# Kernel tuning notes

Hardware: AMD Instinct MI355X
Metric: run time of the kernel (lower is better)

The kernel has to match this reference:

```python
import jax, jax.numpy as jnp
import numpy as np

D_IN, H1, H2, N_CLS, BATCH = 1024, 2048, 2048, 1000, 8192


def setup_inputs() -> dict:
    key = jax.random.key(0)
    ks = jax.random.split(key, 7)
    x = jax.random.normal(ks[0], (BATCH, D_IN), dtype=jnp.float32)
    # torch.nn.Linear default init scale ~ 1/sqrt(fan_in); weights stored [out, in]
    W1 = jax.random.normal(ks[1], (H1, D_IN), dtype=jnp.float32) / np.sqrt(D_IN).astype(np.float32)
    b1 = jax.random.normal(ks[2], (H1,), dtype=jnp.float32) * 0.01
    W2 = jax.random.normal(ks[3], (H2, H1), dtype=jnp.float32) / np.sqrt(H1).astype(np.float32)
    b2 = jax.random.normal(ks[4], (H2,), dtype=jnp.float32) * 0.01
    W3 = jax.random.normal(ks[5], (N_CLS, H2), dtype=jnp.float32) / np.sqrt(H2).astype(np.float32)
    b3 = jax.random.normal(ks[6], (N_CLS,), dtype=jnp.float32) * 0.01
    return {"x": x, "W1": W1, "b1": b1, "W2": W2, "b2": b2, "W3": W3, "b3": b3}


def reference(x, W1, b1, W2, b2, W3, b3):
    # forward_with_coactivations: classifier = [Linear, ReLU, Linear, ReLU, Linear]
    # activation points: the two ReLU layers and the final Linear.
    prev_act = (x > 0).astype(jnp.float32)  # [B, D_IN]

    z1 = x @ W1.T + b1                      # [B, H1]
    a1 = jax.nn.relu(z1)
    act1 = (z1 > 0).astype(jnp.float32)     # (relu(z)>0) == (z>0)
    # sum_s outer(prev_act[s], act1[s]) == prev_act.T @ act1
    coact0 = jnp.einsum('bi,bj->ij', prev_act, act1)  # [D_IN, H1]

    z2 = a1 @ W2.T + b2                     # [B, H2]
    a2 = jax.nn.relu(z2)
    act2 = (z2 > 0).astype(jnp.float32)
    coact1 = jnp.einsum('bi,bj->ij', act1, act2)      # [H1, H2]

    logits = a2 @ W3.T + b3                 # [B, N_CLS]
    act3 = (logits > 0).astype(jnp.float32)
    coact2 = jnp.einsum('bi,bj->ij', act2, act3)      # [H2, N_CLS]

    return logits, coact0, coact1, coact2
```

## Files before the change

### kernel.cpp

```cpp
#include <hip/hip_runtime.h>
#include <hip/hip_bf16.h>


typedef short v8s __attribute__((ext_vector_type(8)));
typedef float v4f __attribute__((ext_vector_type(4)));
typedef int v4i __attribute__((ext_vector_type(4)));

enum { MODE_RELU = 0, MODE_LOGITS = 1 };

__device__ __forceinline__ void async_cp16(const void* gsrc, void* ldst) {
  __builtin_amdgcn_global_load_lds(
      (const __attribute__((address_space(1))) void*)gsrc,
      (__attribute__((address_space(3))) void*)ldst, 16, 0, 0);
}

template <int MODE>
__global__ __launch_bounds__(256) void gemm_nt(
    const __hip_bfloat16* __restrict__ A, const __hip_bfloat16* __restrict__ B,
    const float* __restrict__ bias, void* __restrict__ Cout,
    int M, int N, int K, int n_store, int ldc) {
  __shared__ __hip_bfloat16 sA[128 * 64];
  __shared__ __hip_bfloat16 sB[128 * 64];
  const int t = threadIdx.x;
  const int m0 = blockIdx.y * 128;
  const int n0 = blockIdx.x * 128;

  const __hip_bfloat16* aG[4];
  const __hip_bfloat16* bG[4];
  char* lA[4];
  char* lB[4];
#pragma unroll
  for (int j = 0; j < 4; j++) {
    const int c = j * 256 + t;
    const int row = c >> 3;
    const int g = (c & 7) ^ (row & 7);
    aG[j] = A + (size_t)(m0 + row) * K + g * 8;
    bG[j] = B + (size_t)(n0 + row) * K + g * 8;
    lA[j] = (char*)sA + c * 16;
    lB[j] = (char*)sB + c * 16;
  }

  const int lane = t & 63;
  const int wave = t >> 6;
  const int wm = (wave & 1) * 64;
  const int wn = (wave >> 1) * 64;
  const int lrow = lane & 15;
  const int quad = lane >> 4;

  const int g0 = quad ^ (lrow & 7);
  const __hip_bfloat16* pa0 = sA + (wm + lrow) * 64 + g0 * 8;
  const __hip_bfloat16* pa1 = sA + (wm + lrow) * 64 + (g0 ^ 4) * 8;
  const __hip_bfloat16* pb0 = sB + (wn + lrow) * 64 + g0 * 8;
  const __hip_bfloat16* pb1 = sB + (wn + lrow) * 64 + (g0 ^ 4) * 8;

  v4f acc[4][4] = {};

  for (int k0 = 0; k0 < K; k0 += 64) {
#pragma unroll
    for (int j = 0; j < 4; j++) {
      async_cp16(aG[j] + k0, lA[j]);
      async_cp16(bG[j] + k0, lB[j]);
    }
    __syncthreads();

    v8s a0[4], b0[4], a1[4], b1[4];
#pragma unroll
    for (int i = 0; i < 4; i++) {
      a0[i] = *(const v8s*)(pa0 + i * 16 * 64);
      b0[i] = *(const v8s*)(pb0 + i * 16 * 64);
    }
#pragma unroll
    for (int mi = 0; mi < 4; mi++)
#pragma unroll
      for (int ni = 0; ni < 4; ni++)
        acc[mi][ni] = __builtin_amdgcn_mfma_f32_16x16x32_bf16(
            a0[mi], b0[ni], acc[mi][ni], 0, 0, 0);
#pragma unroll
    for (int i = 0; i < 4; i++) {
      a1[i] = *(const v8s*)(pa1 + i * 16 * 64);
      b1[i] = *(const v8s*)(pb1 + i * 16 * 64);
    }
#pragma unroll
    for (int mi = 0; mi < 4; mi++)
#pragma unroll
      for (int ni = 0; ni < 4; ni++)
        acc[mi][ni] = __builtin_amdgcn_mfma_f32_16x16x32_bf16(
            a1[mi], b1[ni], acc[mi][ni], 0, 0, 0);
    __syncthreads();
  }

#pragma unroll
  for (int ni = 0; ni < 4; ni++) {
    const int col = n0 + wn + ni * 16 + lrow;
    float bv = 0.f;
    if (MODE == MODE_RELU) bv = bias[col];
    if (MODE == MODE_LOGITS && col < n_store) bv = bias[col];
#pragma unroll
    for (int mi = 0; mi < 4; mi++) {
      const int rowb = m0 + wm + mi * 16 + quad * 4;
#pragma unroll
      for (int r = 0; r < 4; r++) {
        const int row = rowb + r;
        const float v = acc[mi][ni][r] + bv;
        if (MODE == MODE_RELU) {
          ((__hip_bfloat16*)Cout)[(size_t)row * ldc + col] =
              __float2bfloat16(v > 0.f ? v : 0.f);
        } else {
          if (col < n_store)
            ((float*)Cout)[(size_t)row * ldc + col] = v;
        }
      }
    }
  }
}

__global__ __launch_bounds__(256) void gemm_nt_i8(
    const char* __restrict__ A, const char* __restrict__ B,
    float* __restrict__ P, int M, int N, int Kc, int n_store, size_t slice) {
  __shared__ char sA[128 * 128];
  __shared__ char sB[128 * 128];
  const int t = threadIdx.x;
  const int m0 = blockIdx.y * 128;
  const int n0 = blockIdx.x * 128;
  const int kbeg = blockIdx.z * Kc;
  const int kend = kbeg + Kc;
  const size_t K = (size_t)Kc * gridDim.z;
  float* __restrict__ Pz = P + (size_t)blockIdx.z * slice;

  const char* aG[4];
  const char* bG[4];
  char* lA[4];
  char* lB[4];
#pragma unroll
  for (int j = 0; j < 4; j++) {
    const int c = j * 256 + t;
    const int row = c >> 3;
    const int g = (c & 7) ^ (row & 7);
    aG[j] = A + (size_t)(m0 + row) * K + g * 16;
    bG[j] = B + (size_t)(n0 + row) * K + g * 16;
    lA[j] = sA + c * 16;
    lB[j] = sB + c * 16;
  }

  const int lane = t & 63;
  const int wave = t >> 6;
  const int wm = (wave & 1) * 64;
  const int wn = (wave >> 1) * 64;
  const int lrow = lane & 15;
  const int quad = lane >> 4;

  const int g0 = quad ^ (lrow & 7);
  const char* pa0 = sA + (wm + lrow) * 128 + g0 * 16;
  const char* pa1 = sA + (wm + lrow) * 128 + (g0 ^ 4) * 16;
  const char* pb0 = sB + (wn + lrow) * 128 + g0 * 16;
  const char* pb1 = sB + (wn + lrow) * 128 + (g0 ^ 4) * 16;

  v4i acc[4][4] = {};

  for (int k0 = kbeg; k0 < kend; k0 += 128) {
#pragma unroll
    for (int j = 0; j < 4; j++) {
      async_cp16(aG[j] + k0, lA[j]);
      async_cp16(bG[j] + k0, lB[j]);
    }
    __syncthreads();

    v4i a0[4], b0[4], a1[4], b1[4];
#pragma unroll
    for (int i = 0; i < 4; i++) {
      a0[i] = *(const v4i*)(pa0 + i * 16 * 128);
      b0[i] = *(const v4i*)(pb0 + i * 16 * 128);
    }
#pragma unroll
    for (int mi = 0; mi < 4; mi++)
#pragma unroll
      for (int ni = 0; ni < 4; ni++)
        acc[mi][ni] = __builtin_amdgcn_mfma_i32_16x16x64_i8(
            a0[mi], b0[ni], acc[mi][ni], 0, 0, 0);
#pragma unroll
    for (int i = 0; i < 4; i++) {
      a1[i] = *(const v4i*)(pa1 + i * 16 * 128);
      b1[i] = *(const v4i*)(pb1 + i * 16 * 128);
    }
#pragma unroll
    for (int mi = 0; mi < 4; mi++)
#pragma unroll
      for (int ni = 0; ni < 4; ni++)
        acc[mi][ni] = __builtin_amdgcn_mfma_i32_16x16x64_i8(
            a1[mi], b1[ni], acc[mi][ni], 0, 0, 0);
    __syncthreads();
  }

#pragma unroll
  for (int ni = 0; ni < 4; ni++) {
    const int col = n0 + wn + ni * 16 + lrow;
    if (col >= n_store) continue;
#pragma unroll
    for (int mi = 0; mi < 4; mi++) {
      const int rowb = m0 + wm + mi * 16 + quad * 4;
#pragma unroll
      for (int r = 0; r < 4; r++) {
        Pz[(size_t)(rowb + r) * n_store + col] = (float)acc[mi][ni][r];
      }
    }
  }
}

template <int Z>
__global__ __launch_bounds__(256) void reduce_part(
    const float* __restrict__ P, float* __restrict__ out, int n4, size_t slice) {
  const int i = blockIdx.x * 256 + threadIdx.x;
  if (i >= n4) return;
  float4 s = ((const float4*)P)[i];
#pragma unroll
  for (int z = 1; z < Z; z++) {
    const float4 v = ((const float4*)(P + (size_t)z * slice))[i];
    s.x += v.x; s.y += v.y; s.z += v.z; s.w += v.w;
  }
  ((float4*)out)[i] = s;
}

__device__ __forceinline__ float tofl(float v) { return v; }
__device__ __forceinline__ float tofl(__hip_bfloat16 v) { return __bfloat162float(v); }

template <typename Tin>
__global__ __launch_bounds__(256) void transpose_bin8(
    const Tin* __restrict__ in, char* __restrict__ out,
    int R, int ldin, int Cphys) {
  __shared__ char tile[64][65];
  const int c0 = blockIdx.x * 64;
  const int r0 = blockIdx.y * 64;
  const int tx = threadIdx.x & 63;
  const int ty = threadIdx.x >> 6;
#pragma unroll
  for (int i = 0; i < 64; i += 4) {
    const int c = c0 + tx;
    const int r = r0 + ty + i;
    float v = 0.f;
    if (c < Cphys) v = tofl(in[(size_t)r * ldin + c]);
    tile[ty + i][tx] = (v > 0.f) ? 1 : 0;
  }
  __syncthreads();
  const int u = threadIdx.x & 15;
  const int cg = threadIdx.x >> 4;
#pragma unroll
  for (int i = 0; i < 64; i += 16) {
    const int col = cg + i;
    char4 v;
    v.x = tile[4 * u + 0][col];
    v.y = tile[4 * u + 1][col];
    v.z = tile[4 * u + 2][col];
    v.w = tile[4 * u + 3][col];
    *(char4*)&out[(size_t)(c0 + col) * R + r0 + 4 * u] = v;
  }
}

struct Cvt4 {
  const float* src[4];
  __hip_bfloat16* dst[4];
  int n4[4];
};
__global__ __launch_bounds__(256) void f32_to_bf16_multi(Cvt4 c) {
  int i = blockIdx.x * 256 + threadIdx.x;
#pragma unroll
  for (int s = 0; s < 4; s++) {
    if (i < c.n4[s]) {
      const float4 v = ((const float4*)c.src[s])[i];
      union { __hip_bfloat16 h[4]; ushort4 u; } cv;
      cv.h[0] = __float2bfloat16(v.x);
      cv.h[1] = __float2bfloat16(v.y);
      cv.h[2] = __float2bfloat16(v.z);
      cv.h[3] = __float2bfloat16(v.w);
      ((ushort4*)c.dst[s])[i] = cv.u;
      return;
    }
    i -= c.n4[s];
  }
}

extern "C" void kernel_launch(void* const* d_in, const int* in_sizes, int n_in,
                              void* d_out, int out_size, void* d_ws, size_t ws_size,
                              hipStream_t stream) {
  const float* x  = (const float*)d_in[0];
  const float* W1 = (const float*)d_in[1];
  const float* b1 = (const float*)d_in[2];
  const float* W2 = (const float*)d_in[3];
  const float* b2 = (const float*)d_in[4];
  const float* W3 = (const float*)d_in[5];
  const float* b3 = (const float*)d_in[6];

  float* logits = (float*)d_out;
  float* coact0 = logits + (size_t)8192 * 1000;
  float* coact1 = coact0 + (size_t)1024 * 2048;
  float* coact2 = coact1 + (size_t)2048 * 2048;

  char* ws = (char*)d_ws;
  size_t off = 0;
  auto alloc = [&](size_t bytes) {
    char* p = ws + off;
    off += (bytes + 255) & ~(size_t)255;
    return p;
  };
  __hip_bfloat16* X   = (__hip_bfloat16*)alloc((size_t)8192 * 1024 * 2);
  __hip_bfloat16* W1b = (__hip_bfloat16*)alloc((size_t)2048 * 1024 * 2);
  __hip_bfloat16* W2b = (__hip_bfloat16*)alloc((size_t)2048 * 2048 * 2);
  __hip_bfloat16* W3b = (__hip_bfloat16*)alloc((size_t)1024 * 2048 * 2);
  __hip_bfloat16* A1  = (__hip_bfloat16*)alloc((size_t)8192 * 2048 * 2);
  __hip_bfloat16* A2  = (__hip_bfloat16*)alloc((size_t)8192 * 2048 * 2);
  char* T0 = (char*)alloc((size_t)1024 * 8192);
  char* T1 = (char*)alloc((size_t)2048 * 8192);
  char* T2 = (char*)A1;
  char* T3 = (char*)A2;
  float* P = (float*)X;

  const dim3 blk(256);

  {
    Cvt4 c;
    c.src[0] = x;  c.dst[0] = X;   c.n4[0] = 8192 * 1024 / 4;
    c.src[1] = W1; c.dst[1] = W1b; c.n4[1] = 2048 * 1024 / 4;
    c.src[2] = W2; c.dst[2] = W2b; c.n4[2] = 2048 * 2048 / 4;
    c.src[3] = W3; c.dst[3] = W3b; c.n4[3] = 1000 * 2048 / 4;
    const int total = c.n4[0] + c.n4[1] + c.n4[2] + c.n4[3];
    f32_to_bf16_multi<<<(total + 255) / 256, blk, 0, stream>>>(c);
  }

  transpose_bin8<float><<<dim3(16, 128), blk, 0, stream>>>(x, T0, 8192, 1024, 1024);

  gemm_nt<MODE_RELU><<<dim3(16, 64), blk, 0, stream>>>(X, W1b, b1, A1,
                                                       8192, 2048, 1024, 2048, 2048);
  transpose_bin8<__hip_bfloat16><<<dim3(32, 128), blk, 0, stream>>>(A1, T1, 8192, 2048, 2048);

  gemm_nt<MODE_RELU><<<dim3(16, 64), blk, 0, stream>>>(A1, W2b, b2, A2,
                                                       8192, 2048, 2048, 2048, 2048);
  transpose_bin8<__hip_bfloat16><<<dim3(32, 128), blk, 0, stream>>>(A2, T2, 8192, 2048, 2048);

  gemm_nt<MODE_LOGITS><<<dim3(8, 64), blk, 0, stream>>>(A2, W3b, b3, logits,
                                                        8192, 1024, 2048, 1000, 1000);
  transpose_bin8<float><<<dim3(16, 128), blk, 0, stream>>>(logits, T3, 8192, 1000, 1000);

  gemm_nt_i8<<<dim3(16, 8, 4), blk, 0, stream>>>(T0, T1, P,
                                                 1024, 2048, 2048, 2048,
                                                 (size_t)1024 * 2048);
  reduce_part<4><<<1024 * 2048 / 4 / 256, blk, 0, stream>>>(
      P, coact0, 1024 * 2048 / 4, (size_t)1024 * 2048);

  gemm_nt_i8<<<dim3(16, 16, 2), blk, 0, stream>>>(T1, T2, P,
                                                  2048, 2048, 4096, 2048,
                                                  (size_t)2048 * 2048);
  reduce_part<2><<<2048 * 2048 / 4 / 256, blk, 0, stream>>>(
      P, coact1, 2048 * 2048 / 4, (size_t)2048 * 2048);

  gemm_nt_i8<<<dim3(8, 16, 4), blk, 0, stream>>>(T2, T3, P,
                                                 2048, 1024, 2048, 1000,
                                                 (size_t)2048 * 1000);
  reduce_part<4><<<2048 * 1000 / 4 / 256, blk, 0, stream>>>(
      P, coact2, 2048 * 1000 / 4, (size_t)2048 * 1000);
}
```

Measured before the change: 466.4 us.

## Fuse binarized activation transpose into GEMM epilogues and deepen split-K

The three GEMM kernels now compute the (z>0) activation bits in their epilogue, transpose them through shared memory and write the int8 transposed masks directly. This removes three standalone transpose_bin8 passes that reread the bf16/fp32 activations. Workspace aliasing is reshuffled so the partial-sum buffer and mask buffers don't collide. Split-K depth for the int8 coactivation GEMMs doubles, which adds more partial-sum traffic and a heavier reduction in exchange for more parallelism.

```diff
diff --git a/kernel.cpp b/kernel.cpp
--- a/kernel.cpp
+++ b/kernel.cpp
@@ -14,13 +14,14 @@
       (__attribute__((address_space(3))) void*)ldst, 16, 0, 0);
 }
 
-template <int MODE>
+template <int MODE, int WT>
 __global__ __launch_bounds__(256) void gemm_nt(
     const __hip_bfloat16* __restrict__ A, const __hip_bfloat16* __restrict__ B,
     const float* __restrict__ bias, void* __restrict__ Cout,
-    int M, int N, int K, int n_store, int ldc) {
-  __shared__ __hip_bfloat16 sA[128 * 64];
-  __shared__ __hip_bfloat16 sB[128 * 64];
+    char* __restrict__ Tout, int M, int N, int K, int n_store, int ldc) {
+  __shared__ char smem[32768];
+  __hip_bfloat16* sA = (__hip_bfloat16*)smem;
+  __hip_bfloat16* sB = (__hip_bfloat16*)(smem + 16384);
   const int t = threadIdx.x;
   const int m0 = blockIdx.y * 128;
   const int n0 = blockIdx.x * 128;
@@ -89,19 +90,25 @@
     __syncthreads();
   }
 
+  float bvv[4];
 #pragma unroll
   for (int ni = 0; ni < 4; ni++) {
     const int col = n0 + wn + ni * 16 + lrow;
-    float bv = 0.f;
-    if (MODE == MODE_RELU) bv = bias[col];
-    if (MODE == MODE_LOGITS && col < n_store) bv = bias[col];
+    bvv[ni] = 0.f;
+    if (MODE == MODE_RELU) bvv[ni] = bias[col];
+    else if (col < n_store) bvv[ni] = bias[col];
+  }
+
+#pragma unroll
+  for (int ni = 0; ni < 4; ni++) {
+    const int col = n0 + wn + ni * 16 + lrow;
 #pragma unroll
     for (int mi = 0; mi < 4; mi++) {
       const int rowb = m0 + wm + mi * 16 + quad * 4;
 #pragma unroll
       for (int r = 0; r < 4; r++) {
         const int row = rowb + r;
-        const float v = acc[mi][ni][r] + bv;
+        const float v = acc[mi][ni][r] + bvv[ni];
         if (MODE == MODE_RELU) {
           ((__hip_bfloat16*)Cout)[(size_t)row * ldc + col] =
               __float2bfloat16(v > 0.f ? v : 0.f);
@@ -111,6 +118,32 @@
         }
       }
     }
+  }
+
+  if (WT) {
+    char* sT = smem;
+#pragma unroll
+    for (int ni = 0; ni < 4; ni++) {
+      const int c = wn + ni * 16 + lrow;
+#pragma unroll
+      for (int mi = 0; mi < 4; mi++) {
+        const int r = wm + mi * 16 + quad * 4;
+        char4 bits;
+        bits.x = (acc[mi][ni][0] + bvv[ni] > 0.f) ? 1 : 0;
+        bits.y = (acc[mi][ni][1] + bvv[ni] > 0.f) ? 1 : 0;
+        bits.z = (acc[mi][ni][2] + bvv[ni] > 0.f) ? 1 : 0;
+        bits.w = (acc[mi][ni][3] + bvv[ni] > 0.f) ? 1 : 0;
+        *(char4*)&sT[c * 144 + r] = bits;
+      }
+    }
+    __syncthreads();
+    const int c2 = t >> 1;
+    const int hf = (t & 1) * 64;
+    char* dst = Tout + (size_t)(n0 + c2) * 8192 + m0 + hf;
+    const char* src = sT + c2 * 144 + hf;
+#pragma unroll
+    for (int j = 0; j < 4; j++)
+      *(int4*)(dst + j * 16) = *(const int4*)(src + j * 16);
   }
 }
 
@@ -220,12 +253,8 @@
   ((float4*)out)[i] = s;
 }
 
-__device__ __forceinline__ float tofl(float v) { return v; }
-__device__ __forceinline__ float tofl(__hip_bfloat16 v) { return __bfloat162float(v); }
-
-template <typename Tin>
-__global__ __launch_bounds__(256) void transpose_bin8(
-    const Tin* __restrict__ in, char* __restrict__ out,
+__global__ __launch_bounds__(256) void transpose_bin8f(
+    const float* __restrict__ in, char* __restrict__ out,
     int R, int ldin, int Cphys) {
   __shared__ char tile[64][65];
   const int c0 = blockIdx.x * 64;
@@ -237,7 +266,7 @@
     const int c = c0 + tx;
     const int r = r0 + ty + i;
     float v = 0.f;
-    if (c < Cphys) v = tofl(in[(size_t)r * ldin + c]);
+    if (c < Cphys) v = in[(size_t)r * ldin + c];
     tile[ty + i][tx] = (v > 0.f) ? 1 : 0;
   }
   __syncthreads();
@@ -309,9 +338,9 @@
   __hip_bfloat16* A2  = (__hip_bfloat16*)alloc((size_t)8192 * 2048 * 2);
   char* T0 = (char*)alloc((size_t)1024 * 8192);
   char* T1 = (char*)alloc((size_t)2048 * 8192);
-  char* T2 = (char*)A1;
-  char* T3 = (char*)A2;
-  float* P = (float*)X;
+  char* T2 = (char*)X;
+  char* T3 = (char*)W2b;
+  float* P = (float*)A1;
 
   const dim3 blk(256);
 
@@ -325,35 +354,32 @@
     f32_to_bf16_multi<<<(total + 255) / 256, blk, 0, stream>>>(c);
   }
 
-  transpose_bin8<float><<<dim3(16, 128), blk, 0, stream>>>(x, T0, 8192, 1024, 1024);
-
-  gemm_nt<MODE_RELU><<<dim3(16, 64), blk, 0, stream>>>(X, W1b, b1, A1,
-                                                       8192, 2048, 1024, 2048, 2048);
-  transpose_bin8<__hip_bfloat16><<<dim3(32, 128), blk, 0, stream>>>(A1, T1, 8192, 2048, 2048);
-
-  gemm_nt<MODE_RELU><<<dim3(16, 64), blk, 0, stream>>>(A1, W2b, b2, A2,
-                                                       8192, 2048, 2048, 2048, 2048);
-  transpose_bin8<__hip_bfloat16><<<dim3(32, 128), blk, 0, stream>>>(A2, T2, 8192, 2048, 2048);
-
-  gemm_nt<MODE_LOGITS><<<dim3(8, 64), blk, 0, stream>>>(A2, W3b, b3, logits,
-                                                        8192, 1024, 2048, 1000, 1000);
-  transpose_bin8<float><<<dim3(16, 128), blk, 0, stream>>>(logits, T3, 8192, 1000, 1000);
-
-  gemm_nt_i8<<<dim3(16, 8, 4), blk, 0, stream>>>(T0, T1, P,
-                                                 1024, 2048, 2048, 2048,
+  transpose_bin8f<<<dim3(16, 128), blk, 0, stream>>>(x, T0, 8192, 1024, 1024);
+
+  gemm_nt<MODE_RELU, 1><<<dim3(16, 64), blk, 0, stream>>>(
+      X, W1b, b1, A1, T1, 8192, 2048, 1024, 2048, 2048);
+
+  gemm_nt<MODE_RELU, 1><<<dim3(16, 64), blk, 0, stream>>>(
+      A1, W2b, b2, A2, T2, 8192, 2048, 2048, 2048, 2048);
+
+  gemm_nt<MODE_LOGITS, 1><<<dim3(8, 64), blk, 0, stream>>>(
+      A2, W3b, b3, logits, T3, 8192, 1024, 2048, 1000, 1000);
+
+  gemm_nt_i8<<<dim3(16, 8, 8), blk, 0, stream>>>(T0, T1, P,
+                                                 1024, 2048, 1024, 2048,
                                                  (size_t)1024 * 2048);
-  reduce_part<4><<<1024 * 2048 / 4 / 256, blk, 0, stream>>>(
+  reduce_part<8><<<1024 * 2048 / 4 / 256, blk, 0, stream>>>(
       P, coact0, 1024 * 2048 / 4, (size_t)1024 * 2048);
 
-  gemm_nt_i8<<<dim3(16, 16, 2), blk, 0, stream>>>(T1, T2, P,
-                                                  2048, 2048, 4096, 2048,
+  gemm_nt_i8<<<dim3(16, 16, 4), blk, 0, stream>>>(T1, T2, P,
+                                                  2048, 2048, 2048, 2048,
                                                   (size_t)2048 * 2048);
-  reduce_part<2><<<2048 * 2048 / 4 / 256, blk, 0, stream>>>(
+  reduce_part<4><<<2048 * 2048 / 4 / 256, blk, 0, stream>>>(
       P, coact1, 2048 * 2048 / 4, (size_t)2048 * 2048);
 
-  gemm_nt_i8<<<dim3(8, 16, 4), blk, 0, stream>>>(T2, T3, P,
-                                                 2048, 1024, 2048, 1000,
+  gemm_nt_i8<<<dim3(8, 16, 8), blk, 0, stream>>>(T2, T3, P,
+                                                 2048, 1024, 1024, 1000,
                                                  (size_t)2048 * 1000);
-  reduce_part<4><<<2048 * 1000 / 4 / 256, blk, 0, stream>>>(
+  reduce_part<8><<<2048 * 1000 / 4 / 256, blk, 0, stream>>>(
       P, coact2, 2048 * 1000 / 4, (size_t)2048 * 1000);
 }
```

After: 476.0 us. +2.0%, slower.
